# Kernel tuning notes

Measured on AMD Instinct MI355X. Metric: run time of the kernel, lower is better.

Reference implementation:

```python
import jax, jax.numpy as jnp
import numpy as np
from jax import lax

EMB, HDIM, OBS_LEN = 64, 64, 8
BATCH, NSCENES, SCENE = 32768, 4096, 8
SEQ_LEN = 12


def setup_inputs() -> dict:
    key = jax.random.key(0)
    ks = jax.random.split(key, 16)
    obs_traj = jax.random.normal(ks[0], (OBS_LEN, BATCH, 2), jnp.float32)
    last_pos = jax.random.normal(ks[1], (BATCH, 2), jnp.float32)
    last_pos_rel = jax.random.normal(ks[2], (BATCH, 2), jnp.float32)
    starts = jnp.arange(NSCENES, dtype=jnp.int32) * SCENE
    seq_start_end = jnp.stack([starts, starts + SCENE], axis=1)  # (NSCENES, 2)
    # spatial_embedding: Linear(2, EMB)
    W_se = jax.random.normal(ks[3], (EMB, 2), jnp.float32) * 0.5
    b_se = jax.random.normal(ks[4], (EMB,), jnp.float32) * 0.1
    # weight-normed convs: w = g * v / ||v||_(in,k) per out-channel, bias init zero
    def conv_params(k, cout, cin, ksz):
        ka, kb = jax.random.split(k)
        std = np.sqrt(4.0 / (ksz * cin))
        v = jax.random.normal(ka, (cout, cin, ksz), jnp.float32) * std
        g = jax.random.uniform(kb, (cout,), jnp.float32, 0.5, 1.5)
        b = jnp.zeros((cout,), jnp.float32)
        return v, g, b
    v1, g1, b1 = conv_params(ks[5], HDIM, EMB, 3)
    v2, g2, b2 = conv_params(ks[6], HDIM // 2, HDIM, 3)
    v3, g3, b3 = conv_params(ks[7], HDIM // 2, HDIM // 2, 3)
    # hidden2pos: Linear(2*HDIM, 2)
    W_hp = jax.random.normal(ks[8], (2, 2 * HDIM), jnp.float32) * 0.05
    b_hp = jax.random.normal(ks[9], (2,), jnp.float32) * 0.05
    return {"obs_traj": obs_traj, "last_pos": last_pos, "last_pos_rel": last_pos_rel,
            "W_se": W_se, "b_se": b_se,
            "v1": v1, "g1": g1, "b1": b1,
            "v2": v2, "g2": g2, "b2": b2,
            "v3": v3, "g3": g3, "b3": b3,
            "W_hp": W_hp, "b_hp": b_hp,
            "seq_start_end": seq_start_end, "seq_len": SEQ_LEN}


def _wn_conv_relu(x, v, g, b):
    # weight-norm: w[o] = g[o] * v[o] / ||v[o]||  (norm over in-channels and kernel)
    norm = jnp.sqrt(jnp.sum(v * v, axis=(1, 2)))
    w = v * (g / norm)[:, None, None]
    y = lax.conv_general_dilated(x, w, (1,), 'VALID',
                                 dimension_numbers=('NCH', 'OIH', 'NCH'))
    return jax.nn.relu(y + b[None, :, None])


def reference(obs_traj, last_pos, last_pos_rel,
              W_se, b_se, v1, g1, b1, v2, g2, b2, v3, g3, b3, W_hp, b_hp,
              seq_start_end, seq_len):
    batch = last_pos.shape[0]
    nseg = seq_start_end.shape[0]
    h_dim = v1.shape[0]
    # scene id for each pedestrian (segments are contiguous [start,end) ranges)
    seg = jnp.searchsorted(seq_start_end[:, 0], jnp.arange(batch), side='right') - 1
    # obs_traj embedding -> (batch, EMB, OBS_LEN)
    emb = obs_traj @ W_se.T + b_se            # (T, B, EMB)
    obs_emb0 = jnp.transpose(emb, (1, 2, 0))  # (B, EMB, T)

    def step(carry, _):
        obs_emb, lp = carry
        s = _wn_conv_relu(obs_emb, v1, g1, b1)   # (B, H, T-2)
        s = _wn_conv_relu(s, v2, g2, b2)         # (B, H/2, T-4)
        s = _wn_conv_relu(s, v3, g3, b3)         # (B, H/2, T-6)
        s = s.reshape(batch, h_dim)              # (H/2)*(T-6) == H
        mx = jax.ops.segment_max(s, seg, num_segments=nseg)  # ragged per-scene max
        st = jnp.concatenate([s, mx[seg]], axis=1)           # (B, 2H)
        rel = st @ W_hp.T + b_hp                 # (B, 2)
        lp = rel + lp
        dec = rel @ W_se.T + b_se                # (B, EMB)
        obs_emb = jnp.concatenate([obs_emb[:, :, 1:], dec[:, :, None]], axis=2)
        return (obs_emb, lp), rel

    _, rels = lax.scan(step, (obs_emb0, last_pos), None, length=seq_len)
    return rels  # (seq_len, batch, 2)
```

## Files before the change

kernel.cpp:

```cpp
#include <hip/hip_runtime.h>

#define BATCH 32768
#define SEQLEN 12
#define NBLK 512

typedef short short8 __attribute__((ext_vector_type(8)));
typedef float f32x4 __attribute__((ext_vector_type(4)));
typedef unsigned short ushort_t;

static __device__ __forceinline__ unsigned short f2bf(float x) {
    unsigned u = __float_as_uint(x);
    return (unsigned short)((u + 0x7FFFu + ((u >> 16) & 1u)) >> 16);
}
static __device__ __forceinline__ float bf2f(unsigned short h) {
    return __uint_as_float(((unsigned)h) << 16);
}

#define MFMA __builtin_amdgcn_mfma_f32_16x16x32_bf16

#define FMAXDPP(X, CTRL) \
    fmaxf((X), __int_as_float(__builtin_amdgcn_mov_dpp(__float_as_int(X), (CTRL), 0xF, 0xF, true)))


#define CONV1D(PA_, PB_, R0_, R1_, SL_) do {                                  \
    _Pragma("unroll")                                                         \
    for (int ich_ = 0; ich_ < 2; ++ich_) {                                    \
        const int cb_ = ich_*32 + kg*8;                                       \
        short8 sh_, sl_;                                                      \
        _Pragma("unroll")                                                     \
        for (int j_ = 0; j_ < 8; ++j_) {                                      \
            float4 c0_ = *(const float4*)&c1t8[cb_ + j_][0];                  \
            float4 c1_ = *(const float4*)&c1t8[cb_ + j_][4];                  \
            float v_ = c1_.z;                                         \
            v_ = fmaf(c0_.x, (PA_).x, v_); v_ = fmaf(c0_.y, (PA_).y, v_);     \
            v_ = fmaf(c0_.z, (PB_).x, v_); v_ = fmaf(c0_.w, (PB_).y, v_);     \
            v_ = fmaf(c1_.x, (R0_), v_);   v_ = fmaf(c1_.y, (R1_), v_);       \
            v_ = fmaxf(v_, 0.f);                                              \
            ushort_t h_ = f2bf(v_);                                           \
            sh_[j_] = (short)h_;                                              \
            sl_[j_] = (short)f2bf(v_ - bf2f(h_));                             \
        }                                                                     \
        s1fh[SL_][ich_] = sh_; s1fl[SL_][ich_] = sl_;                         \
    }                                                                         \
} while(0)

#define WCONV1D(SA_, SB_, SC_, SL_) do {                                      \
    float2 pa_ = *(const float2*)&pos_s[wv][SA_][n][0];                       \
    float2 pb_ = *(const float2*)&pos_s[wv][SB_][n][0];                       \
    float2 pc_ = *(const float2*)&pos_s[wv][SC_][n][0];                       \
    CONV1D(pa_, pb_, pc_.x, pc_.y, SL_);                                      \
} while(0)

#define CONV2COL(CM3) do {                                                    \
    const float* b2b_ = &b2s[0];                                              \
    asm volatile("" : "+v"(b2b_));                                            \
    _Pragma("unroll")                                                         \
    for (int T = 0; T < 2; ++T) {                                             \
        f32x4 a1 = {0.f,0.f,0.f,0.f}, a2 = {0.f,0.f,0.f,0.f},                 \
              a3 = {0.f,0.f,0.f,0.f};                                         \
        _Pragma("unroll")                                                     \
        for (int kb = 0; kb < 6; ++kb) {                                      \
            const int sl = ((CM3) + (kb >> 1)) % 3, ich = kb & 1;             \
            const short8 wh = *(const short8*)&c2wh[T*6+kb][lane][0];         \
            const short8 wl = *(const short8*)&c2wl[T*6+kb][lane][0];         \
            a1 = MFMA(wh, s1fh[sl][ich], a1, 0, 0, 0);                        \
            a2 = MFMA(wh, s1fl[sl][ich], a2, 0, 0, 0);                        \
            a3 = MFMA(wl, s1fh[sl][ich], a3, 0, 0, 0);                        \
        }                                                                     \
        const float4 bb = *(const float4*)&b2b_[T*16 + kg*4];                 \
        float w0 = fmaxf(a1[0]+a2[0]+a3[0]+bb.x, 0.f);                        \
        float w1 = fmaxf(a1[1]+a2[1]+a3[1]+bb.y, 0.f);                        \
        float w2 = fmaxf(a1[2]+a2[2]+a3[2]+bb.z, 0.f);                        \
        float w3 = fmaxf(a1[3]+a2[3]+a3[3]+bb.w, 0.f);                        \
        ushort_t h0=f2bf(w0), h1=f2bf(w1), h2=f2bf(w2), h3=f2bf(w3);          \
        *(uint2*)&s2sh[wv][n][T*16 + kg*4] = make_uint2(                      \
            (unsigned)h0 | ((unsigned)h1 << 16),                              \
            (unsigned)h2 | ((unsigned)h3 << 16));                             \
        *(uint2*)&s2sl[wv][n][T*16 + kg*4] = make_uint2(                      \
            (unsigned)f2bf(w0-bf2f(h0)) | ((unsigned)f2bf(w1-bf2f(h1)) << 16),\
            (unsigned)f2bf(w2-bf2f(h2)) | ((unsigned)f2bf(w3-bf2f(h3)) << 16));\
    }                                                                         \
    s2fh[(CM3)] = *(const short8*)&s2sh[wv][n][kg*8];                         \
    s2fl[(CM3)] = *(const short8*)&s2sl[wv][n][kg*8];                         \
} while(0)

#define CONV3COL(VM3, PARI) do {                                              \
    const float* b3b_ = &b3s[0];                                              \
    asm volatile("" : "+v"(b3b_));                                            \
    _Pragma("unroll")                                                         \
    for (int T = 0; T < 2; ++T) {                                             \
        f32x4 a1 = {0.f,0.f,0.f,0.f}, a2 = {0.f,0.f,0.f,0.f},                 \
              a3 = {0.f,0.f,0.f,0.f};                                         \
        _Pragma("unroll")                                                     \
        for (int kb = 0; kb < 3; ++kb) {                                      \
            const int sl = ((VM3) + kb) % 3;                                  \
            const short8 wh = *(const short8*)&c3wh[T*3+kb][lane][0];         \
            a1 = MFMA(wh, s2fh[sl], a1, 0, 0, 0);                             \
            a2 = MFMA(wh, s2fl[sl], a2, 0, 0, 0);                             \
            a3 = MFMA(c3l[T][kb], s2fh[sl], a3, 0, 0, 0);                     \
        }                                                                     \
        const float4 b3v = *(const float4*)&b3b_[T*16 + kg*4];                \
        float m0 = fmaxf(a1[0]+a2[0]+a3[0]+b3v.x, 0.f);                       \
        float m1 = fmaxf(a1[1]+a2[1]+a3[1]+b3v.y, 0.f);                       \
        float m2 = fmaxf(a1[2]+a2[2]+a3[2]+b3v.z, 0.f);                       \
        float m3 = fmaxf(a1[3]+a2[3]+a3[3]+b3v.w, 0.f);                       \
        c3c[PARI][T] = (f32x4){m0, m1, m2, m3};                               \
        m0 = FMAXDPP(m0, 0xB1); m0 = FMAXDPP(m0, 0x4E); m0 = FMAXDPP(m0, 0x141);\
        m1 = FMAXDPP(m1, 0xB1); m1 = FMAXDPP(m1, 0x4E); m1 = FMAXDPP(m1, 0x141);\
        m2 = FMAXDPP(m2, 0xB1); m2 = FMAXDPP(m2, 0x4E); m2 = FMAXDPP(m2, 0x141);\
        m3 = FMAXDPP(m3, 0xB1); m3 = FMAXDPP(m3, 0x4E); m3 = FMAXDPP(m3, 0x141);\
        mxc[PARI][T] = (f32x4){m0, m1, m2, m3};                               \
    }                                                                         \
} while(0)

#define STAGE2(T0) do {                                                       \
    const int tau_ = (T0) + (lane >> 5);                                      \
    const int p_ = (lane >> 1) & 15, c_ = lane & 1;                           \
    pos_s[wv][tau_ & 3][p_][c_] =                                             \
        obs[(size_t)(tau_*BATCH + bped + p_)*2 + c_];                         \
} while(0)

#define STEP(K) do {                                                          \
    const int st = sbase + (K);                                               \
    float2 c1pa = *(const float2*)&pos_s[wv][(st+2)&3][n][0];                 \
    float2 c1pb = *(const float2*)&pos_s[wv][(st+3)&3][n][0];                 \
    float pv0a = 0.f, pv0b = 0.f, pv1a = 0.f, pv1b = 0.f;                     \
    {                                                                         \
        const float* wqf_ = &whp_s[kg][0];                                    \
        asm volatile("" : "+v"(wqf_));     \
        const float4* wq = (const float4*)wqf_;                               \
        _Pragma("unroll")                                                     \
        for (int q = 0; q < 16; ++q) {                                        \
            float4 ww = wq[q];                                                \
            _Pragma("unroll")                                                 \
            for (int e = 0; e < 4; ++e) {                                     \
                const int j2 = (q & 7)*4 + e;                                 \
                const int jj = j2 & 15;                                       \
                const int T = jj >> 3, r = (jj >> 1) & 3, col = jj & 1;       \
                const int par = col ? (((K)+1) & 1) : ((K) & 1);              \
                float val = (j2 < 16) ? c3c[par][T][r] : mxc[par][T][r];      \
                float wv_ = (e==0)?ww.x:(e==1)?ww.y:(e==2)?ww.z:ww.w;         \
                if (q < 8) { if (q & 1) pv0b = fmaf(wv_, val, pv0b);          \
                             else       pv0a = fmaf(wv_, val, pv0a); }        \
                else       { if (q & 1) pv1b = fmaf(wv_, val, pv1b);          \
                             else       pv1a = fmaf(wv_, val, pv1a); }        \
            }                                                                 \
        }                                                                     \
    }                                                                         \
    float pv0 = pv0a + pv0b, pv1 = pv1a + pv1b;                               \
    pv0 += __shfl_xor(pv0, 16); pv0 += __shfl_xor(pv0, 32);                   \
    pv1 += __shfl_xor(pv1, 16); pv1 += __shfl_xor(pv1, 32);                   \
    const float r0 = pv0 + bhp0, r1 = pv1 + bhp1;                             \
    if (lane < 16) {                                                          \
        float2 o; o.x = r0; o.y = r1;                                         \
        *(float2*)&out[(size_t)(st*BATCH + bped + lane)*2] = o;               \
    }                                                                         \
    if (st < SEQLEN-1) {                                                      \
        if (lane < 16) {                                                      \
            float2 o2; o2.x = r0; o2.y = r1;                                  \
            *(float2*)&pos_s[wv][st & 3][lane][0] = o2;         \
        }                                                                     \
        CONV1D(c1pa, c1pb, r0, r1, (K)%3);                      \
        CONV2COL(((K)+1)%3);                                    \
        CONV3COL(((K)+2)%3, (K)&1);                             \
    }                                                                         \
} while(0)

__global__ __launch_bounds__(256, 2)
void enc_wp(const float* __restrict__ obs,
            const float* __restrict__ Wse, const float* __restrict__ bse,
            const float* __restrict__ v1, const float* __restrict__ g1, const float* __restrict__ b1,
            const float* __restrict__ v2, const float* __restrict__ g2, const float* __restrict__ b2,
            const float* __restrict__ v3, const float* __restrict__ g3, const float* __restrict__ b3,
            const float* __restrict__ Whp, const float* __restrict__ bhp,
            float* __restrict__ out)
{
    __shared__ __align__(16) ushort_t s2sh[4][16][40], s2sl[4][16][40];
    __shared__ __align__(16) float    pos_s[4][4][16][2];
    __shared__ __align__(16) float    whp_s[4][68];
    __shared__ __align__(16) ushort_t c2wh[12][64][8], c2wl[12][64][8];
    __shared__ __align__(16) ushort_t c3wh[6][64][8];
    __shared__ __align__(16) float    b2s[32], b3s[32];
    __shared__ __align__(16) float    c1t8[64][8];

    const int tid  = threadIdx.x;
    const int wv   = tid >> 6;
    const int lane = tid & 63;
    const int n    = lane & 15, kg = lane >> 4;
    const int bped = (blockIdx.x*4 + wv)*16;

    float* scr   = (float*)&s2sh[0][0][0];
    float* wse_s = scr;
    float* bse_s = scr + 128;
    float* sc2_s = scr + 192;
    float* sc3_s = scr + 224;

    if (wv == 0) {
        wse_s[lane] = Wse[lane]; wse_s[64 + lane] = Wse[64 + lane];
        bse_s[lane] = bse[lane];
        if (lane < 32) {
            b2s[lane] = b2[lane];
            const float* v = v2 + lane*192; float s = 0.f;
            for (int j = 0; j < 192; ++j) s += v[j]*v[j];
            sc2_s[lane] = g2[lane] / sqrtf(s);
        } else {
            b3s[lane-32] = b3[lane-32];
            const float* v = v3 + (lane-32)*96; float s = 0.f;
            for (int j = 0; j < 96; ++j) s += v[j]*v[j];
            sc3_s[lane-32] = g3[lane-32] / sqrtf(s);
        }
        #pragma unroll
        for (int q = 0; q < 4; ++q) {
            int d = lane >> 5, jp = lane & 31, jj = jp & 15;
            int T = jj >> 3, r = (jj >> 1) & 3, col = jj & 1;
            int off = (T*16 + q*4 + r)*2 + col + ((jp >= 16) ? 64 : 0);
            whp_s[q][lane] = Whp[d*128 + off];
        }
    }
    __syncthreads();

    if (wv == 0) {
        const float* v = v1 + lane*192; float s = 0.f;
        for (int j = 0; j < 192; ++j) s += v[j]*v[j];
        const float sc1 = g1[lane] / sqrtf(s);
        float dA0=0,dA1=0,dA2=0,dB0=0,dB1=0,dB2=0,dC0=0,dC1=0,dC2=0;
        const float* vr = v1 + lane*192;
        #pragma unroll 4
        for (int ic = 0; ic < 64; ++ic) {
            float w0 = vr[ic*3], w1 = vr[ic*3+1], w2 = vr[ic*3+2];
            float we0 = wse_s[ic*2], we1 = wse_s[ic*2+1], be = bse_s[ic];
            dA0 = fmaf(w0, we0, dA0); dB0 = fmaf(w0, we1, dB0); dC0 = fmaf(w0, be, dC0);
            dA1 = fmaf(w1, we0, dA1); dB1 = fmaf(w1, we1, dB1); dC1 = fmaf(w1, be, dC1);
            dA2 = fmaf(w2, we0, dA2); dB2 = fmaf(w2, we1, dB2); dC2 = fmaf(w2, be, dC2);
        }
        c1t8[lane][0] = sc1*dA0; c1t8[lane][1] = sc1*dB0;
        c1t8[lane][2] = sc1*dA1; c1t8[lane][3] = sc1*dB1;
        c1t8[lane][4] = sc1*dA2; c1t8[lane][5] = sc1*dB2;
        c1t8[lane][6] = fmaf(sc1, (dC0 + dC1) + dC2, b1[lane]);
        c1t8[lane][7] = 0.f;
    } else if (wv == 2) {
        #pragma unroll
        for (int f = 0; f < 12; ++f) {
            const int T = f / 6, kb = f % 6;
            const int oc = T*16 + n, tap = kb >> 1, ich = kb & 1;
            const float s2s = sc2_s[oc];
            #pragma unroll
            for (int j = 0; j < 8; ++j) {
                const int ic = ich*32 + kg*8 + j;
                float w = v2[(size_t)(oc*64 + ic)*3 + tap] * s2s;
                ushort_t hb = f2bf(w);
                c2wh[f][lane][j] = hb;
                c2wl[f][lane][j] = f2bf(w - bf2f(hb));
            }
        }
    } else if (wv == 1) {
        #pragma unroll
        for (int f = 0; f < 6; ++f) {
            const int T = f / 3, kb = f % 3;
            const int oc = T*16 + n;
            const float s3s = sc3_s[oc];
            #pragma unroll
            for (int j = 0; j < 8; ++j) {
                const int ic = kg*8 + j;
                c3wh[f][lane][j] = f2bf(v3[(size_t)(oc*32 + ic)*3 + kb] * s3s);
            }
        }
    }
    short8 c3l[2][3];
    #pragma unroll
    for (int T = 0; T < 2; ++T) {
        const int oc = T*16 + n;
        const float s3s = sc3_s[oc];
        #pragma unroll
        for (int kb = 0; kb < 3; ++kb) {
            #pragma unroll
            for (int j = 0; j < 8; ++j) {
                const int ic = kg*8 + j;
                float w = v3[(size_t)(oc*32 + ic)*3 + kb] * s3s;
                c3l[T][kb][j] = (short)f2bf(w - bf2f(f2bf(w)));
            }
        }
    }
    const float bhp0 = bhp[0], bhp1 = bhp[1];
    __syncthreads();

    short8 s1fh[3][2], s1fl[3][2], s2fh[3], s2fl[3];
    f32x4 c3c[2][2], mxc[2][2];

    STAGE2(0); STAGE2(2);
    WCONV1D(0, 1, 2, 0);
    WCONV1D(1, 2, 3, 1);
    STAGE2(4);
    WCONV1D(2, 3, 0, 2);
    CONV2COL(0);
    WCONV1D(3, 0, 1, 0);
    CONV2COL(1);
    STAGE2(6);
    WCONV1D(0, 1, 2, 1);
    CONV2COL(2);
    CONV3COL(0, 0);
    WCONV1D(1, 2, 3, 2);
    CONV2COL(0);
    CONV3COL(1, 1);

    #pragma unroll 1
    for (int hh = 0; hh < 2; ++hh) {
        const int sbase = hh * 6;
        STEP(0); STEP(1); STEP(2); STEP(3); STEP(4); STEP(5);
    }
}

extern "C" void kernel_launch(void* const* d_in, const int* in_sizes, int n_in,
                              void* d_out, int out_size, void* d_ws, size_t ws_size,
                              hipStream_t stream)
{
    const float* obs = (const float*)d_in[0];
    const float* Wse = (const float*)d_in[3];
    const float* bse = (const float*)d_in[4];
    const float* v1  = (const float*)d_in[5];
    const float* g1  = (const float*)d_in[6];
    const float* b1  = (const float*)d_in[7];
    const float* v2  = (const float*)d_in[8];
    const float* g2  = (const float*)d_in[9];
    const float* b2  = (const float*)d_in[10];
    const float* v3  = (const float*)d_in[11];
    const float* g3  = (const float*)d_in[12];
    const float* b3  = (const float*)d_in[13];
    const float* Whp = (const float*)d_in[14];
    const float* bhp = (const float*)d_in[15];

    enc_wp<<<NBLK, 256, 0, stream>>>(obs, Wse, bse, v1, g1, b1, v2, g2, b2,
                                     v3, g3, b3, Whp, bhp, (float*)d_out);
}
```

Measured before the change: 176.6 us.

## Halve block size, keep hi-bf16 conv weights in registers, split conv1 into base+finish

Blocks shrink from 4 to 2 waves and the grid doubles, so per-block setup is split across 128 threads. The high-precision bf16 halves of the conv2 and conv3 weights now live in registers, and only the low halves stay in shared memory, which cuts LDS traffic and LDS footprint. Conv1 is split so the part that depends on already-known positions is computed before the hidden2pos dot product, leaving only two FMAs per channel on the critical path. The cost is more registers per thread and duplicated weight setup across twice as many blocks.

After: 241.0 us. 36.4% more time.

```diff
diff --git a/kernel.cpp b/kernel.cpp
--- a/kernel.cpp
+++ b/kernel.cpp
@@ -2,7 +2,7 @@
 
 #define BATCH 32768
 #define SEQLEN 12
-#define NBLK 512
+#define NBLK 1024
 
 typedef short short8 __attribute__((ext_vector_type(8)));
 typedef float f32x4 __attribute__((ext_vector_type(4)));
@@ -22,33 +22,70 @@
     fmaxf((X), __int_as_float(__builtin_amdgcn_mov_dpp(__float_as_int(X), (CTRL), 0xF, 0xF, true)))
 
 
-#define CONV1D(PA_, PB_, R0_, R1_, SL_) do {                                  \
+#define F4FMA(ACC, X, S) do {                                                 \
+    (ACC).x = fmaf((X).x, (S), (ACC).x); (ACC).y = fmaf((X).y, (S), (ACC).y); \
+    (ACC).z = fmaf((X).z, (S), (ACC).z); (ACC).w = fmaf((X).w, (S), (ACC).w); \
+} while(0)
+
+#define C1BASE(PA_, PB_) do {                                                 \
     _Pragma("unroll")                                                         \
     for (int ich_ = 0; ich_ < 2; ++ich_) {                                    \
-        const int cb_ = ich_*32 + kg*8;                                       \
+        const float* ct_ = &c1t7[0][ich_*32 + kg*8];                          \
+        float4 aL_ = *(const float4*)(ct_ + 6*64);                            \
+        float4 aH_ = *(const float4*)(ct_ + 6*64 + 4);                        \
+        float4 xL_ = *(const float4*)(ct_ + 0*64);                            \
+        float4 xH_ = *(const float4*)(ct_ + 0*64 + 4);                        \
+        F4FMA(aL_, xL_, (PA_).x); F4FMA(aH_, xH_, (PA_).x);                   \
+        xL_ = *(const float4*)(ct_ + 1*64); xH_ = *(const float4*)(ct_ + 1*64 + 4); \
+        F4FMA(aL_, xL_, (PA_).y); F4FMA(aH_, xH_, (PA_).y);                   \
+        xL_ = *(const float4*)(ct_ + 2*64); xH_ = *(const float4*)(ct_ + 2*64 + 4); \
+        F4FMA(aL_, xL_, (PB_).x); F4FMA(aH_, xH_, (PB_).x);                   \
+        xL_ = *(const float4*)(ct_ + 3*64); xH_ = *(const float4*)(ct_ + 3*64 + 4); \
+        F4FMA(aL_, xL_, (PB_).y); F4FMA(aH_, xH_, (PB_).y);                   \
+        baseL[ich_] = aL_; baseH[ich_] = aH_;                                 \
+    }                                                                         \
+} while(0)
+
+#define C1FIN(R0_, R1_, SL_) do {                                             \
+    _Pragma("unroll")                                                         \
+    for (int ich_ = 0; ich_ < 2; ++ich_) {                                    \
+        const float* ct_ = &c1t7[0][ich_*32 + kg*8];                          \
+        float4 a2L_ = *(const float4*)(ct_ + 4*64);                           \
+        float4 a2H_ = *(const float4*)(ct_ + 4*64 + 4);                       \
+        float4 b2L_ = *(const float4*)(ct_ + 5*64);                           \
+        float4 b2H_ = *(const float4*)(ct_ + 5*64 + 4);                       \
         short8 sh_, sl_;                                                      \
         _Pragma("unroll")                                                     \
-        for (int j_ = 0; j_ < 8; ++j_) {                                      \
-            float4 c0_ = *(const float4*)&c1t8[cb_ + j_][0];                  \
-            float4 c1_ = *(const float4*)&c1t8[cb_ + j_][4];                  \
-            float v_ = c1_.z;                                         \
-            v_ = fmaf(c0_.x, (PA_).x, v_); v_ = fmaf(c0_.y, (PA_).y, v_);     \
-            v_ = fmaf(c0_.z, (PB_).x, v_); v_ = fmaf(c0_.w, (PB_).y, v_);     \
-            v_ = fmaf(c1_.x, (R0_), v_);   v_ = fmaf(c1_.y, (R1_), v_);       \
+        for (int j_ = 0; j_ < 4; ++j_) {                                      \
+            float v_ = fmaf(((const float*)&a2L_)[j_], (R0_),                 \
+                            ((const float*)&baseL[ich_])[j_]);                \
+            v_ = fmaf(((const float*)&b2L_)[j_], (R1_), v_);                  \
             v_ = fmaxf(v_, 0.f);                                              \
             ushort_t h_ = f2bf(v_);                                           \
             sh_[j_] = (short)h_;                                              \
             sl_[j_] = (short)f2bf(v_ - bf2f(h_));                             \
         }                                                                     \
+        _Pragma("unroll")                                                     \
+        for (int j_ = 0; j_ < 4; ++j_) {                                      \
+            float v_ = fmaf(((const float*)&a2H_)[j_], (R0_),                 \
+                            ((const float*)&baseH[ich_])[j_]);                \
+            v_ = fmaf(((const float*)&b2H_)[j_], (R1_), v_);                  \
+            v_ = fmaxf(v_, 0.f);                                              \
+            ushort_t h_ = f2bf(v_);                                           \
+            sh_[4+j_] = (short)h_;                                            \
+            sl_[4+j_] = (short)f2bf(v_ - bf2f(h_));                           \
+        }                                                                     \
         s1fh[SL_][ich_] = sh_; s1fl[SL_][ich_] = sl_;                         \
     }                                                                         \
 } while(0)
 
-#define WCONV1D(SA_, SB_, SC_, SL_) do {                                      \
+#define C1FULL(SA_, SB_, SC_, SL_) do {                                       \
     float2 pa_ = *(const float2*)&pos_s[wv][SA_][n][0];                       \
     float2 pb_ = *(const float2*)&pos_s[wv][SB_][n][0];                       \
     float2 pc_ = *(const float2*)&pos_s[wv][SC_][n][0];                       \
-    CONV1D(pa_, pb_, pc_.x, pc_.y, SL_);                                      \
+    float4 baseL[2], baseH[2];                                                \
+    C1BASE(pa_, pb_);                                                         \
+    C1FIN(pc_.x, pc_.y, SL_);                                                 \
 } while(0)
 
 #define CONV2COL(CM3) do {                                                    \
@@ -61,10 +98,9 @@
         _Pragma("unroll")                                                     \
         for (int kb = 0; kb < 6; ++kb) {                                      \
             const int sl = ((CM3) + (kb >> 1)) % 3, ich = kb & 1;             \
-            const short8 wh = *(const short8*)&c2wh[T*6+kb][lane][0];         \
             const short8 wl = *(const short8*)&c2wl[T*6+kb][lane][0];         \
-            a1 = MFMA(wh, s1fh[sl][ich], a1, 0, 0, 0);                        \
-            a2 = MFMA(wh, s1fl[sl][ich], a2, 0, 0, 0);                        \
+            a1 = MFMA(c2h[T][kb], s1fh[sl][ich], a1, 0, 0, 0);                \
+            a2 = MFMA(c2h[T][kb], s1fl[sl][ich], a2, 0, 0, 0);                \
             a3 = MFMA(wl, s1fh[sl][ich], a3, 0, 0, 0);                        \
         }                                                                     \
         const float4 bb = *(const float4*)&b2b_[T*16 + kg*4];                 \
@@ -94,10 +130,10 @@
         _Pragma("unroll")                                                     \
         for (int kb = 0; kb < 3; ++kb) {                                      \
             const int sl = ((VM3) + kb) % 3;                                  \
-            const short8 wh = *(const short8*)&c3wh[T*3+kb][lane][0];         \
-            a1 = MFMA(wh, s2fh[sl], a1, 0, 0, 0);                             \
-            a2 = MFMA(wh, s2fl[sl], a2, 0, 0, 0);                             \
-            a3 = MFMA(c3l[T][kb], s2fh[sl], a3, 0, 0, 0);                     \
+            const short8 wl = *(const short8*)&c3wl[T*3+kb][lane][0];         \
+            a1 = MFMA(c3h[T][kb], s2fh[sl], a1, 0, 0, 0);                     \
+            a2 = MFMA(c3h[T][kb], s2fl[sl], a2, 0, 0, 0);                     \
+            a3 = MFMA(wl, s2fh[sl], a3, 0, 0, 0);                             \
         }                                                                     \
         const float4 b3v = *(const float4*)&b3b_[T*16 + kg*4];                \
         float m0 = fmaxf(a1[0]+a2[0]+a3[0]+b3v.x, 0.f);                       \
@@ -124,6 +160,8 @@
     const int st = sbase + (K);                                               \
     float2 c1pa = *(const float2*)&pos_s[wv][(st+2)&3][n][0];                 \
     float2 c1pb = *(const float2*)&pos_s[wv][(st+3)&3][n][0];                 \
+    float4 baseL[2], baseH[2];                                                \
+    C1BASE(c1pa, c1pb);            \
     float pv0a = 0.f, pv0b = 0.f, pv1a = 0.f, pv1b = 0.f;                     \
     {                                                                         \
         const float* wqf_ = &whp_s[kg][0];                                    \
@@ -160,13 +198,13 @@
             float2 o2; o2.x = r0; o2.y = r1;                                  \
             *(float2*)&pos_s[wv][st & 3][lane][0] = o2;         \
         }                                                                     \
-        CONV1D(c1pa, c1pb, r0, r1, (K)%3);                      \
+        C1FIN(r0, r1, (K)%3);                                   \
         CONV2COL(((K)+1)%3);                                    \
         CONV3COL(((K)+2)%3, (K)&1);                             \
     }                                                                         \
 } while(0)
 
-__global__ __launch_bounds__(256, 2)
+__global__ __launch_bounds__(128, 2)
 void enc_wp(const float* __restrict__ obs,
             const float* __restrict__ Wse, const float* __restrict__ bse,
             const float* __restrict__ v1, const float* __restrict__ g1, const float* __restrict__ b1,
@@ -175,47 +213,47 @@
             const float* __restrict__ Whp, const float* __restrict__ bhp,
             float* __restrict__ out)
 {
-    __shared__ __align__(16) ushort_t s2sh[4][16][40], s2sl[4][16][40];
-    __shared__ __align__(16) float    pos_s[4][4][16][2];
+    __shared__ __align__(16) ushort_t c2wl[12][64][8];
+    __shared__ __align__(16) ushort_t c3wl[6][64][8];
+    __shared__ __align__(16) ushort_t s2sh[2][16][40], s2sl[2][16][40];
+    __shared__ __align__(16) float    pos_s[2][4][16][2];
     __shared__ __align__(16) float    whp_s[4][68];
-    __shared__ __align__(16) ushort_t c2wh[12][64][8], c2wl[12][64][8];
-    __shared__ __align__(16) ushort_t c3wh[6][64][8];
+    __shared__ __align__(16) float    c1t7[7][64];
     __shared__ __align__(16) float    b2s[32], b3s[32];
-    __shared__ __align__(16) float    c1t8[64][8];
 
     const int tid  = threadIdx.x;
     const int wv   = tid >> 6;
     const int lane = tid & 63;
     const int n    = lane & 15, kg = lane >> 4;
-    const int bped = (blockIdx.x*4 + wv)*16;
-
-    float* scr   = (float*)&s2sh[0][0][0];
-    float* wse_s = scr;
-    float* bse_s = scr + 128;
-    float* sc2_s = scr + 192;
-    float* sc3_s = scr + 224;
-
-    if (wv == 0) {
-        wse_s[lane] = Wse[lane]; wse_s[64 + lane] = Wse[64 + lane];
-        bse_s[lane] = bse[lane];
-        if (lane < 32) {
-            b2s[lane] = b2[lane];
-            const float* v = v2 + lane*192; float s = 0.f;
-            for (int j = 0; j < 192; ++j) s += v[j]*v[j];
-            sc2_s[lane] = g2[lane] / sqrtf(s);
-        } else {
-            b3s[lane-32] = b3[lane-32];
-            const float* v = v3 + (lane-32)*96; float s = 0.f;
-            for (int j = 0; j < 96; ++j) s += v[j]*v[j];
-            sc3_s[lane-32] = g3[lane-32] / sqrtf(s);
-        }
+    const int bped = (blockIdx.x*2 + wv)*16;
+
+    float* wse_s = (float*)&s2sh[0][0][0];
+    float* bse_s = wse_s + 128;
+    float* sc2_s = (float*)&s2sl[0][0][0];
+    float* sc3_s = sc2_s + 32;
+
+    wse_s[tid] = Wse[tid];
+    if (tid < 64) {
+        bse_s[tid] = bse[tid];
         #pragma unroll
         for (int q = 0; q < 4; ++q) {
-            int d = lane >> 5, jp = lane & 31, jj = jp & 15;
+            int d = tid >> 5, jp = tid & 31, jj = jp & 15;
             int T = jj >> 3, r = (jj >> 1) & 3, col = jj & 1;
             int off = (T*16 + q*4 + r)*2 + col + ((jp >= 16) ? 64 : 0);
-            whp_s[q][lane] = Whp[d*128 + off];
-        }
+            whp_s[q][tid] = Whp[d*128 + off];
+        }
+    } else if (tid < 96) {
+        const int i = tid - 64;
+        b2s[i] = b2[i];
+        const float* v = v2 + i*192; float s = 0.f;
+        for (int j = 0; j < 192; ++j) s += v[j]*v[j];
+        sc2_s[i] = g2[i] / sqrtf(s);
+    } else {
+        const int i = tid - 96;
+        b3s[i] = b3[i];
+        const float* v = v3 + i*96; float s = 0.f;
+        for (int j = 0; j < 96; ++j) s += v[j]*v[j];
+        sc3_s[i] = g3[i] / sqrtf(s);
     }
     __syncthreads();
 
@@ -233,12 +271,11 @@
             dA1 = fmaf(w1, we0, dA1); dB1 = fmaf(w1, we1, dB1); dC1 = fmaf(w1, be, dC1);
             dA2 = fmaf(w2, we0, dA2); dB2 = fmaf(w2, we1, dB2); dC2 = fmaf(w2, be, dC2);
         }
-        c1t8[lane][0] = sc1*dA0; c1t8[lane][1] = sc1*dB0;
-        c1t8[lane][2] = sc1*dA1; c1t8[lane][3] = sc1*dB1;
-        c1t8[lane][4] = sc1*dA2; c1t8[lane][5] = sc1*dB2;
-        c1t8[lane][6] = fmaf(sc1, (dC0 + dC1) + dC2, b1[lane]);
-        c1t8[lane][7] = 0.f;
-    } else if (wv == 2) {
+        c1t7[0][lane] = sc1*dA0; c1t7[1][lane] = sc1*dB0;
+        c1t7[2][lane] = sc1*dA1; c1t7[3][lane] = sc1*dB1;
+        c1t7[4][lane] = sc1*dA2; c1t7[5][lane] = sc1*dB2;
+        c1t7[6][lane] = fmaf(sc1, (dC0 + dC1) + dC2, b1[lane]);
+    } else {
         #pragma unroll
         for (int f = 0; f < 12; ++f) {
             const int T = f / 6, kb = f % 6;
@@ -248,12 +285,9 @@
             for (int j = 0; j < 8; ++j) {
                 const int ic = ich*32 + kg*8 + j;
                 float w = v2[(size_t)(oc*64 + ic)*3 + tap] * s2s;
-                ushort_t hb = f2bf(w);
-                c2wh[f][lane][j] = hb;
-                c2wl[f][lane][j] = f2bf(w - bf2f(hb));
+                c2wl[f][lane][j] = f2bf(w - bf2f(f2bf(w)));
             }
         }
-    } else if (wv == 1) {
         #pragma unroll
         for (int f = 0; f < 6; ++f) {
             const int T = f / 3, kb = f % 3;
@@ -262,11 +296,27 @@
             #pragma unroll
             for (int j = 0; j < 8; ++j) {
                 const int ic = kg*8 + j;
-                c3wh[f][lane][j] = f2bf(v3[(size_t)(oc*32 + ic)*3 + kb] * s3s);
+                float w = v3[(size_t)(oc*32 + ic)*3 + kb] * s3s;
+                c3wl[f][lane][j] = f2bf(w - bf2f(f2bf(w)));
             }
         }
     }
-    short8 c3l[2][3];
+    short8 c2h[2][6];
+    #pragma unroll
+    for (int T = 0; T < 2; ++T) {
+        const int oc2 = T*16 + n;
+        const float s2s = sc2_s[oc2];
+        #pragma unroll
+        for (int kb = 0; kb < 6; ++kb) {
+            const int tap = kb >> 1, ich = kb & 1;
+            #pragma unroll
+            for (int j = 0; j < 8; ++j) {
+                const int ic = ich*32 + kg*8 + j;
+                c2h[T][kb][j] = (short)f2bf(v2[(size_t)(oc2*64 + ic)*3 + tap] * s2s);
+            }
+        }
+    }
+    short8 c3h[2][3];
     #pragma unroll
     for (int T = 0; T < 2; ++T) {
         const int oc = T*16 + n;
@@ -276,8 +326,7 @@
             #pragma unroll
             for (int j = 0; j < 8; ++j) {
                 const int ic = kg*8 + j;
-                float w = v3[(size_t)(oc*32 + ic)*3 + kb] * s3s;
-                c3l[T][kb][j] = (short)f2bf(w - bf2f(f2bf(w)));
+                c3h[T][kb][j] = (short)f2bf(v3[(size_t)(oc*32 + ic)*3 + kb] * s3s);
             }
         }
     }
@@ -288,18 +337,18 @@
     f32x4 c3c[2][2], mxc[2][2];
 
     STAGE2(0); STAGE2(2);
-    WCONV1D(0, 1, 2, 0);
-    WCONV1D(1, 2, 3, 1);
+    C1FULL(0, 1, 2, 0);
+    C1FULL(1, 2, 3, 1);
     STAGE2(4);
-    WCONV1D(2, 3, 0, 2);
+    C1FULL(2, 3, 0, 2);
     CONV2COL(0);
-    WCONV1D(3, 0, 1, 0);
+    C1FULL(3, 0, 1, 0);
     CONV2COL(1);
     STAGE2(6);
-    WCONV1D(0, 1, 2, 1);
+    C1FULL(0, 1, 2, 1);
     CONV2COL(2);
     CONV3COL(0, 0);
-    WCONV1D(1, 2, 3, 2);
+    C1FULL(1, 2, 3, 2);
     CONV2COL(0);
     CONV3COL(1, 1);
 
@@ -329,6 +378,6 @@
     const float* Whp = (const float*)d_in[14];
     const float* bhp = (const float*)d_in[15];
 
-    enc_wp<<<NBLK, 256, 0, stream>>>(obs, Wse, bse, v1, g1, b1, v2, g2, b2,
+    enc_wp<<<NBLK, 128, 0, stream>>>(obs, Wse, bse, v1, g1, b1, v2, g2, b2,
                                      v3, g3, b3, Whp, bhp, (float*)d_out);
 }
```
